# Optimization experiments

Hardware: AMD Instinct MI355X
Metric: run time of the kernel (lower is better)

The kernel has to match this reference:

```python
import jax, jax.numpy as jnp
import numpy as np

N_QUBITS = 4
N_LAYERS = 2
DIM = 1 << N_QUBITS  # 16-dim state vector

# --- fixed (parameter-free) CNOT entangler layers, precomputed as 16x16 permutations ---

def _cnot_perm(c, t):
    M = np.zeros((DIM, DIM), np.complex64)
    for b in range(DIM):
        b2 = b ^ (1 << (N_QUBITS - 1 - t)) if (b >> (N_QUBITS - 1 - c)) & 1 else b
        M[b2, b] = 1.0
    return M

def _entangler(r):
    E = np.eye(DIM, dtype=np.complex64)
    for i in range(N_QUBITS):  # pennylane applies CNOT(i, (i+r)%n) sequentially
        E = _cnot_perm(i, (i + r) % N_QUBITS) @ E
    return E

ENT = [jnp.asarray(_entangler((l % (N_QUBITS - 1)) + 1)) for l in range(N_LAYERS)]
# Z_TABLE[b, w] = <b| Z_w |b>
Z_TABLE = jnp.asarray(np.array([[1.0 - 2.0 * ((b >> (N_QUBITS - 1 - w)) & 1) for w in range(N_QUBITS)] for b in range(DIM)], np.float32))


def _rot(phi, theta, omega):
    # pennylane Rot = RZ(omega) @ RY(theta) @ RZ(phi)
    c = jnp.cos(theta / 2).astype(jnp.complex64)
    s = jnp.sin(theta / 2).astype(jnp.complex64)
    a = jnp.exp(-0.5j * (phi + omega)) * c
    b = -jnp.exp(0.5j * (phi - omega)) * s
    cc = jnp.exp(-0.5j * (phi - omega)) * s
    d = jnp.exp(0.5j * (phi + omega)) * c
    return jnp.stack([jnp.stack([a, b]), jnp.stack([cc, d])])


def _vqc_unitary(weights):
    # weights: [N_LAYERS, N_QUBITS, 3] -> 16x16 unitary for StronglyEntanglingLayers
    U = jnp.eye(DIM, dtype=jnp.complex64)
    for l in range(N_LAYERS):
        R = _rot(weights[l, 0, 0], weights[l, 0, 1], weights[l, 0, 2])
        for q in range(1, N_QUBITS):  # wire 0 is most-significant bit -> left kron factor
            R = jnp.kron(R, _rot(weights[l, q, 0], weights[l, q, 1], weights[l, q, 2]))
        U = ENT[l] @ (R @ U)
    return U


def _vqc(x, weights):
    # x: [..., 4] rotation angles; AngleEmbedding uses RX: RX(a)|0> = [cos(a/2), -i sin(a/2)]
    c = jnp.cos(x / 2).astype(jnp.complex64)
    s = jnp.sin(x / 2).astype(jnp.complex64)
    amp = jnp.stack([c, -1j * s], axis=-1)  # [..., 4, 2]
    psi0 = jnp.einsum('...a,...b,...c,...d->...abcd', amp[..., 0, :], amp[..., 1, :], amp[..., 2, :], amp[..., 3, :])
    psi0 = psi0.reshape(x.shape[:-1] + (DIM,))
    U = _vqc_unitary(weights)
    psi = jnp.einsum('ij,...j->...i', U, psi0)
    probs = psi.real ** 2 + psi.imag ** 2
    return probs @ Z_TABLE  # [..., 4] PauliZ expectation values


def setup_inputs() -> dict:
    key = jax.random.key(0)
    k0, k1, k2, k3 = jax.random.split(key, 4)
    H = 768
    B, S = 8, 2048
    embeddings = jax.random.normal(k0, (B, S, H), dtype=jnp.float32)
    lim = 1.0 / np.sqrt(H)
    Wq = jax.random.normal(k1, (N_QUBITS, H), dtype=jnp.float32) * lim
    Wk = jax.random.normal(k2, (N_QUBITS, H), dtype=jnp.float32) * lim
    bq = jnp.zeros((N_QUBITS,), jnp.float32)
    bk = jnp.zeros((N_QUBITS,), jnp.float32)
    vqc_weights = jax.random.uniform(k3, (N_LAYERS, N_QUBITS, 3), dtype=jnp.float32) * (2.0 * np.pi)
    return {'embeddings': embeddings, 'Wq': Wq, 'bq': bq, 'Wk': Wk, 'bk': bk, 'vqc_weights': vqc_weights}


def reference(embeddings, Wq, bq, Wk, bk, vqc_weights):
    Q = jnp.einsum('bsh,qh->bsq', embeddings, Wq) + bq  # [B,S,4]
    K = jnp.einsum('bsh,qh->bsq', embeddings, Wk) + bk
    Qv = _vqc(Q, vqc_weights)  # [B,S,4]
    Kv = _vqc(K, vqc_weights)
    attn = jax.nn.softmax(jnp.einsum('bsq,btq->bst', Qv, Kv), axis=-1)  # [B,S,S]
    return jnp.einsum('bst,bth->bsh', attn, embeddings)
```

## Files before the change

kernel.cpp:

```cpp
#include <hip/hip_runtime.h>

#define NB 8
#define NS 2048
#define NH 768
#define NPOS (NB*NS)

typedef short short8 __attribute__((ext_vector_type(8)));
typedef float floatx4 __attribute__((ext_vector_type(4)));

__device__ __forceinline__ unsigned pack_bf16(unsigned b0, unsigned b1) {
  return __builtin_amdgcn_perm(b1, b0, 0x07060302u);
}

#define GLOAD_LDS16(gp, lp) __builtin_amdgcn_global_load_lds( \
  (const __attribute__((address_space(1))) unsigned int*)(gp), \
  (__attribute__((address_space(3))) unsigned int*)(lp), 16, 0, 0)

__global__ void build_V_kernel(const float* __restrict__ wts,
                               float* __restrict__ Vre, float* __restrict__ Vim) {
  int j = threadIdx.x;
  if (j >= 16) return;
  float ar[16], ai[16];
#pragma unroll
  for (int i = 0; i < 16; i++) { ar[i] = (i == j) ? 1.f : 0.f; ai[i] = 0.f; }
#pragma unroll
  for (int l = 0; l < 2; l++) {
#pragma unroll
    for (int q = 0; q < 4; q++) {
      float phi = wts[(l*4+q)*3+0];
      float th  = wts[(l*4+q)*3+1];
      float om  = wts[(l*4+q)*3+2];
      float ct = cosf(0.5f*th), st = sinf(0.5f*th);
      float sm = 0.5f*(phi+om), df = 0.5f*(phi-om);
      float cs = cosf(sm), ss = sinf(sm), cd = cosf(df), sd = sinf(df);
      float Ar =  cs*ct, Ai = -ss*ct;
      float Br = -cd*st, Bi = -sd*st;
      float Cr =  cd*st, Ci = -sd*st;
      float Dr =  cs*ct, Di =  ss*ct;
      int pb = 1 << (3-q);
#pragma unroll
      for (int b0 = 0; b0 < 16; b0++) {
        if (b0 & pb) continue;
        int b1 = b0 | pb;
        float xr = ar[b0], xi = ai[b0], yr = ar[b1], yi = ai[b1];
        ar[b0] = Ar*xr - Ai*xi + Br*yr - Bi*yi;
        ai[b0] = Ar*xi + Ai*xr + Br*yi + Bi*yr;
        ar[b1] = Cr*xr - Ci*xi + Dr*yr - Di*yi;
        ai[b1] = Cr*xi + Ci*xr + Dr*yi + Di*yr;
      }
    }
    const int r = (l == 0) ? 1 : 2;
#pragma unroll
    for (int i2 = 0; i2 < 4; i2++) {
      int cb = 1 << (3-i2);
      int tb = 1 << (3-((i2+r)&3));
#pragma unroll
      for (int b0 = 0; b0 < 16; b0++) {
        if ((b0 & cb) && !(b0 & tb)) {
          int b1 = b0 | tb;
          float tr = ar[b0], ti = ai[b0];
          ar[b0] = ar[b1]; ai[b0] = ai[b1];
          ar[b1] = tr;     ai[b1] = ti;
        }
      }
    }
  }
  int pc = __popc((unsigned)j) & 3;
#pragma unroll
  for (int i = 0; i < 16; i++) {
    float vr = ar[i], vi = ai[i], orr, oi;
    if      (pc == 0) { orr =  vr; oi =  vi; }
    else if (pc == 1) { orr =  vi; oi = -vr; }
    else if (pc == 2) { orr = -vr; oi = -vi; }
    else              { orr = -vi; oi =  vr; }
    Vre[i*16+j] = orr;
    Vim[i*16+j] = oi;
  }
}

__global__ __launch_bounds__(256) void proj_vqc_kernel(
    const float* __restrict__ E, const float* __restrict__ Wq, const float* __restrict__ bq,
    const float* __restrict__ Wk, const float* __restrict__ bk,
    const float* __restrict__ Vre, const float* __restrict__ Vim,
    float* __restrict__ Qv, float* __restrict__ Kv) {
  __shared__ __align__(16) float WqL[768*4];
  __shared__ __align__(16) float WkL[768*4];
  __shared__ float Vsh[2][16*17];
  int tid = threadIdx.x;
  for (int idx = tid; idx < 768*4; idx += 256) {
    int e = idx >> 2, w = idx & 3;
    WqL[e*4+w] = Wq[w*768+e];
    WkL[e*4+w] = Wk[w*768+e];
  }
  if (tid < 256) {
    int i = tid >> 4, jj = tid & 15;
    Vsh[0][i*17+jj] = Vre[tid];
    Vsh[1][i*17+jj] = Vim[tid];
  }
  __syncthreads();
  float bqr0=bq[0], bqr1=bq[1], bqr2=bq[2], bqr3=bq[3];
  float bkr0=bk[0], bkr1=bk[1], bkr2=bk[2], bkr3=bk[3];
  int lane = tid & 63;
  int wid  = blockIdx.x*4 + (tid >> 6);
  int nw   = gridDim.x*4;
  int grp  = lane >> 4;
  int i    = lane & 15;
  for (int pos = wid; pos < NPOS; pos += nw) {
    const float* er = E + (size_t)pos*768;
    float pq[4] = {0.f,0.f,0.f,0.f};
    float pk[4] = {0.f,0.f,0.f,0.f};
#pragma unroll
    for (int k2 = 0; k2 < 3; k2++) {
      float4 ev = *(const float4*)(er + lane*4 + 256*k2);
#pragma unroll
      for (int jj = 0; jj < 4; jj++) {
        int e = lane*4 + 256*k2 + jj;
        float evs = (jj==0) ? ev.x : (jj==1) ? ev.y : (jj==2) ? ev.z : ev.w;
        float4 wq4 = *(const float4*)&WqL[e*4];
        float4 wk4 = *(const float4*)&WkL[e*4];
        pq[0] += evs*wq4.x; pq[1] += evs*wq4.y; pq[2] += evs*wq4.z; pq[3] += evs*wq4.w;
        pk[0] += evs*wk4.x; pk[1] += evs*wk4.y; pk[2] += evs*wk4.z; pk[3] += evs*wk4.w;
      }
    }
    float part[8];
#pragma unroll
    for (int w = 0; w < 8; w++) {
      float v = (w < 4) ? pq[w] : pk[w-4];
      v += __shfl_xor(v, 32); v += __shfl_xor(v, 16); v += __shfl_xor(v, 8);
      v += __shfl_xor(v, 4);  v += __shfl_xor(v, 2);  v += __shfl_xor(v, 1);
      part[w] = v;
    }
    if (grp < 2) {
      float a0,a1,a2,a3;
      if (grp == 0) { a0=part[0]+bqr0; a1=part[1]+bqr1; a2=part[2]+bqr2; a3=part[3]+bqr3; }
      else          { a0=part[4]+bkr0; a1=part[5]+bkr1; a2=part[6]+bkr2; a3=part[7]+bkr3; }
      float c0=cosf(0.5f*a0), s0=sinf(0.5f*a0);
      float c1=cosf(0.5f*a1), s1=sinf(0.5f*a1);
      float c2=cosf(0.5f*a2), s2=sinf(0.5f*a2);
      float c3=cosf(0.5f*a3), s3=sinf(0.5f*a3);
      float m[16];
#pragma unroll
      for (int j2 = 0; j2 < 16; j2++) {
        float f0 = (j2 & 8) ? s0 : c0;
        float f1 = (j2 & 4) ? s1 : c1;
        float f2 = (j2 & 2) ? s2 : c2;
        float f3 = (j2 & 1) ? s3 : c3;
        m[j2] = f0*f1*f2*f3;
      }
      float re = 0.f, im = 0.f;
#pragma unroll
      for (int j2 = 0; j2 < 16; j2++) {
        re += Vsh[0][i*17+j2]*m[j2];
        im += Vsh[1][i*17+j2]*m[j2];
      }
      float pr = re*re + im*im;
      float r0 = (i & 8) ? -pr : pr;
      float r1 = (i & 4) ? -pr : pr;
      float r2 = (i & 2) ? -pr : pr;
      float r3 = (i & 1) ? -pr : pr;
#pragma unroll
      for (int off = 8; off >= 1; off >>= 1) {
        r0 += __shfl_xor(r0, off);
        r1 += __shfl_xor(r1, off);
        r2 += __shfl_xor(r2, off);
        r3 += __shfl_xor(r3, off);
      }
      if (i == 0) {
        float* dst = (grp == 0 ? Qv : Kv) + (size_t)pos*4;
        dst[0]=r0; dst[1]=r1; dst[2]=r2; dst[3]=r3;
      }
    }
  }
}

__global__ __launch_bounds__(256) void epre_kernel(
    const float* __restrict__ E, unsigned short* __restrict__ EhiT,
    unsigned short* __restrict__ EloT) {
  int tc = blockIdx.x, hb = blockIdx.y, b = blockIdx.z;
  size_t tbase = ((size_t)((b*6 + hb)*64 + tc)) * 4096;
  const float* Eb = E + (size_t)b*NS*NH + (size_t)tc*32*NH + hb*128;
  int tid = threadIdx.x;
#pragma unroll
  for (int u = 0; u < 2; u++) {
    int unit = tid + 256*u;
    int h2 = unit & 127, q2 = unit >> 7;
    unsigned hi4[4], lo4[4];
#pragma unroll
    for (int jp = 0; jp < 4; jp++) {
      float ea = Eb[(size_t)(q2*8 + 2*jp    )*NH + h2];
      float eb = Eb[(size_t)(q2*8 + 2*jp + 1)*NH + h2];
      unsigned ba = __float_as_uint(ea), bb = __float_as_uint(eb);
      float la = ea - __uint_as_float(ba & 0xFFFF0000u);
      float lb = eb - __uint_as_float(bb & 0xFFFF0000u);
      hi4[jp] = pack_bf16(ba, bb);
      lo4[jp] = pack_bf16(__float_as_uint(la), __float_as_uint(lb));
    }
    int off = h2*32 + ((q2 ^ ((h2>>1)&3))*8);
    *(uint4*)&EhiT[tbase + off] = make_uint4(hi4[0],hi4[1],hi4[2],hi4[3]);
    *(uint4*)&EloT[tbase + off] = make_uint4(lo4[0],lo4[1],lo4[2],lo4[3]);
  }
}

#define BS 128
#define BH 128
#define TK 32

__global__ __launch_bounds__(256, 3) void attn_kernel(
    const float* __restrict__ E, const float* __restrict__ Qv,
    const float* __restrict__ Kv, const unsigned short* __restrict__ EhiT,
    const unsigned short* __restrict__ EloT, float* __restrict__ out) {
  int sblk = blockIdx.x;
  int hblk = blockIdx.y;
  int b    = blockIdx.z;
  int tid  = threadIdx.x;
  int lane = tid & 63;
  int w    = tid >> 6;

  __shared__ __align__(16) unsigned short sAhi[BS*TK];
  __shared__ __align__(16) unsigned short sAlo[BS*TK];
  __shared__ __align__(16) unsigned short sBhi[2][BH*TK];
  __shared__ __align__(16) unsigned short sBlo[2][BH*TK];
  __shared__ __align__(16) float kvf[2][TK][4];
  __shared__ float denp[BS*4];
  __shared__ float dfin[BS];

  const float* Kvb = Kv + (size_t)b*NS*4;
  const unsigned short* tHi = EhiT + ((size_t)(b*6 + hblk)*64) * 4096;
  const unsigned short* tLo = EloT + ((size_t)(b*6 + hblk)*64) * 4096;

  int qw = w, sL = lane;
  floatx4 qv0, qv1;
  {
    const float4 t0 = *(const float4*)&Qv[((size_t)(b*NS + sblk*BS) + sL)*4];
    const float4 t1 = *(const float4*)&Qv[((size_t)(b*NS + sblk*BS) + 64 + sL)*4];
    qv0 = floatx4{t0.x, t0.y, t0.z, t0.w};
    qv1 = floatx4{t1.x, t1.y, t1.z, t1.w};
  }
  float den0 = 0.f, den1 = 0.f;

  int sh = w & 1, hh = w >> 1;
  floatx4 acc[4][4];
#pragma unroll
  for (int i = 0; i < 4; i++)
#pragma unroll
    for (int jt = 0; jt < 4; jt++) acc[i][jt] = floatx4{0.f,0.f,0.f,0.f};

  int m16 = lane & 15, q16 = lane >> 4;
  int cidx = (q16 ^ ((m16 >> 1) & 3)) * 8;

  GLOAD_LDS16(tHi + (size_t)tid*8,        &sBhi[0][tid*8]);
  GLOAD_LDS16(tHi + 2048 + (size_t)tid*8, &sBhi[0][2048 + tid*8]);
  GLOAD_LDS16(tLo + (size_t)tid*8,        &sBlo[0][tid*8]);
  GLOAD_LDS16(tLo + 2048 + (size_t)tid*8, &sBlo[0][2048 + tid*8]);
  if (tid < 32) GLOAD_LDS16(Kvb + tid*4, &kvf[0][0][0] + tid*4);

  for (int tc = 0; tc < NS; tc += TK) {
    int cb = (tc >> 5) & 1;
    __syncthreads();

    {
      unsigned hiA[2][4], loA[2][4];
#pragma unroll
      for (int jp = 0; jp < 4; jp++) {
        float4 ka = *(const float4*)&kvf[cb][qw*8 + 2*jp][0];
        float4 kb = *(const float4*)&kvf[cb][qw*8 + 2*jp + 1][0];
#pragma unroll
        for (int r = 0; r < 2; r++) {
          floatx4 qv = r ? qv1 : qv0;
          float arga = qv.x*ka.x + qv.y*ka.y + qv.z*ka.z + qv.w*ka.w;
          float argb = qv.x*kb.x + qv.y*kb.y + qv.z*kb.z + qv.w*kb.w;
          float pa = __expf(arga), pb = __expf(argb);
          if (r) den1 += pa + pb; else den0 += pa + pb;
          unsigned bpa = __float_as_uint(pa), bpb = __float_as_uint(pb);
          float lpa = pa - __uint_as_float(bpa & 0xFFFF0000u);
          float lpb = pb - __uint_as_float(bpb & 0xFFFF0000u);
          hiA[r][jp] = pack_bf16(bpa, bpb);
          loA[r][jp] = pack_bf16(__float_as_uint(lpa), __float_as_uint(lpb));
        }
      }
#pragma unroll
      for (int r = 0; r < 2; r++) {
        int s = sL + 64*r;
        int off = s*TK + ((qw ^ ((s>>1)&3))*8);
        *(uint4*)&sAhi[off] = make_uint4(hiA[r][0],hiA[r][1],hiA[r][2],hiA[r][3]);
        *(uint4*)&sAlo[off] = make_uint4(loA[r][0],loA[r][1],loA[r][2],loA[r][3]);
      }
    }

    __syncthreads();

    if (tc + TK < NS) {
      int nb = cb ^ 1;
      const unsigned short* nHi = tHi + (size_t)((tc >> 5) + 1) * 4096;
      const unsigned short* nLo = tLo + (size_t)((tc >> 5) + 1) * 4096;
      GLOAD_LDS16(nHi + (size_t)tid*8,        &sBhi[nb][tid*8]);
      GLOAD_LDS16(nHi + 2048 + (size_t)tid*8, &sBhi[nb][2048 + tid*8]);
      GLOAD_LDS16(nLo + (size_t)tid*8,        &sBlo[nb][tid*8]);
      GLOAD_LDS16(nLo + 2048 + (size_t)tid*8, &sBlo[nb][2048 + tid*8]);
      if (tid < 32) GLOAD_LDS16(Kvb + (size_t)(tc+TK)*4 + tid*4, &kvf[nb][0][0] + tid*4);
    }

    short8 bh_[4], bl_[4];
#pragma unroll
    for (int jt = 0; jt < 4; jt++) {
      int hrow = hh*64 + jt*16 + m16;
      bh_[jt] = __builtin_bit_cast(short8, *(const uint4*)&sBhi[cb][hrow*TK + cidx]);
      bl_[jt] = __builtin_bit_cast(short8, *(const uint4*)&sBlo[cb][hrow*TK + cidx]);
    }
#pragma unroll
    for (int i = 0; i < 4; i++) {
      int srow = sh*64 + i*16 + m16;
      short8 ah = __builtin_bit_cast(short8, *(const uint4*)&sAhi[srow*TK + cidx]);
      short8 al = __builtin_bit_cast(short8, *(const uint4*)&sAlo[srow*TK + cidx]);
#pragma unroll
      for (int jt = 0; jt < 4; jt++) {
        acc[i][jt] = __builtin_amdgcn_mfma_f32_16x16x32_bf16(ah, bl_[jt], acc[i][jt], 0, 0, 0);
        acc[i][jt] = __builtin_amdgcn_mfma_f32_16x16x32_bf16(al, bh_[jt], acc[i][jt], 0, 0, 0);
        acc[i][jt] = __builtin_amdgcn_mfma_f32_16x16x32_bf16(ah, bh_[jt], acc[i][jt], 0, 0, 0);
      }
    }
  }

  __syncthreads();
  denp[sL*4 + qw] = den0;
  denp[(64 + sL)*4 + qw] = den1;
  __syncthreads();
  if (tid < BS) {
    dfin[tid] = denp[tid*4] + denp[tid*4+1] + denp[tid*4+2] + denp[tid*4+3];
  }
  __syncthreads();

  float* ob = out + ((size_t)(b*NS + sblk*BS))*NH + hblk*BH;
#pragma unroll
  for (int i = 0; i < 4; i++) {
#pragma unroll
    for (int reg = 0; reg < 4; reg++) {
      int row = q16*4 + reg;
      int s_loc = sh*64 + i*16 + row;
      float invd = 1.0f / dfin[s_loc];
#pragma unroll
      for (int jt = 0; jt < 4; jt++) {
        int h_loc = hh*64 + jt*16 + m16;
        ob[(size_t)s_loc*NH + h_loc] = acc[i][jt][reg] * invd;
      }
    }
  }
}

extern "C" void kernel_launch(void* const* d_in, const int* in_sizes, int n_in,
                              void* d_out, int out_size, void* d_ws, size_t ws_size,
                              hipStream_t stream) {
  const float* E   = (const float*)d_in[0];
  const float* Wq  = (const float*)d_in[1];
  const float* bq  = (const float*)d_in[2];
  const float* Wk  = (const float*)d_in[3];
  const float* bk  = (const float*)d_in[4];
  const float* wts = (const float*)d_in[5];
  float* ws  = (float*)d_ws;
  float* Vre = ws;
  float* Vim = ws + 256;
  float* Qv  = ws + 512;
  float* Kv  = ws + 512 + NPOS*4;
  unsigned short* EhiT = (unsigned short*)(ws + 512 + 2*NPOS*4);
  unsigned short* EloT = EhiT + (size_t)NB*6*64*4096;
  float* out = (float*)d_out;

  build_V_kernel<<<1, 64, 0, stream>>>(wts, Vre, Vim);
  epre_kernel<<<dim3(64, 6, 8), 256, 0, stream>>>(E, EhiT, EloT);
  proj_vqc_kernel<<<1024, 256, 0, stream>>>(E, Wq, bq, Wk, bk, Vre, Vim, Qv, Kv);
  attn_kernel<<<dim3(16, 6, 8), 256, 0, stream>>>(E, Qv, Kv, EhiT, EloT, out);
}
```

Baseline: 323.2 us.

## Precompute softmax numerators once in a separate kernel instead of per H-block

The attention kernel used to recompute exp(Q·K) scores and their bf16 hi/lo split for every one of the six H-blocks. A new pgen_kernel now computes the split probability tiles once, stores them to global memory in the swizzled MFMA layout, and accumulates softmax denominators with atomics after a memset. The attention kernel then streams both the P and E tiles through LDS with async global-to-LDS loads and reorders the MFMA loop so A fragments are held in registers. This trades redundant exp/ALU work for a large extra global write and repeated reads of the P buffer, plus more workspace and an extra launch and memset.

```diff
diff --git a/kernel.cpp b/kernel.cpp
--- a/kernel.cpp
+++ b/kernel.cpp
@@ -201,43 +201,81 @@
   }
 }
 
-#define BS 128
-#define BH 128
-#define TK 32
+__global__ __launch_bounds__(256) void pgen_kernel(
+    const float* __restrict__ Qv, const float* __restrict__ Kv,
+    unsigned short* __restrict__ PhiT, unsigned short* __restrict__ PloT,
+    float* __restrict__ den) {
+  int tq = blockIdx.x, sblk = blockIdx.y, b = blockIdx.z;
+  int tid = threadIdx.x;
+  __shared__ __align__(16) float kvl[256*4];
+  {
+    const float4 v = ((const float4*)(Kv + ((size_t)b*NS + tq*256)*4))[tid];
+    ((float4*)kvl)[tid ^ ((tid >> 3) & 3)] = v;
+  }
+  int s0 = tid >> 2, c = tid & 3;
+  const float* Qb = Qv + ((size_t)b*NS + sblk*128)*4;
+  float4 qv0 = *(const float4*)&Qb[s0*4];
+  float4 qv1 = *(const float4*)&Qb[(64+s0)*4];
+  __syncthreads();
+  float den0 = 0.f, den1 = 0.f;
+  size_t tb = ((size_t)((b*16 + sblk)*64) + tq*8) * 4096;
+  int off0 = s0*32 + ((c ^ ((s0>>1)&3))*8);
+  int off1 = (64+s0)*32 + ((c ^ (((64+s0)>>1)&3))*8);
+#pragma unroll 2
+  for (int tt = 0; tt < 8; tt++) {
+#pragma unroll
+    for (int r = 0; r < 2; r++) {
+      float4 qv = r ? qv1 : qv0;
+      unsigned hi4[4], lo4[4];
+      float dsum = 0.f;
+#pragma unroll
+      for (int jp = 0; jp < 4; jp++) {
+        int La = tt*32 + c*8 + 2*jp;
+        float4 ka = ((const float4*)kvl)[La ^ c];
+        float4 kb = ((const float4*)kvl)[(La+1) ^ c];
+        float arga = qv.x*ka.x + qv.y*ka.y + qv.z*ka.z + qv.w*ka.w;
+        float argb = qv.x*kb.x + qv.y*kb.y + qv.z*kb.z + qv.w*kb.w;
+        float pa = __expf(arga), pb = __expf(argb);
+        dsum += pa + pb;
+        unsigned bpa = __float_as_uint(pa), bpb = __float_as_uint(pb);
+        float lpa = pa - __uint_as_float(bpa & 0xFFFF0000u);
+        float lpb = pb - __uint_as_float(bpb & 0xFFFF0000u);
+        hi4[jp] = pack_bf16(bpa, bpb);
+        lo4[jp] = pack_bf16(__float_as_uint(lpa), __float_as_uint(lpb));
+      }
+      if (r) den1 += dsum; else den0 += dsum;
+      size_t base = tb + (size_t)tt*4096 + (r ? off1 : off0);
+      *(uint4*)&PhiT[base] = make_uint4(hi4[0],hi4[1],hi4[2],hi4[3]);
+      *(uint4*)&PloT[base] = make_uint4(lo4[0],lo4[1],lo4[2],lo4[3]);
+    }
+  }
+  atomicAdd(&den[(size_t)b*NS + sblk*128 + s0], den0);
+  atomicAdd(&den[(size_t)b*NS + sblk*128 + 64 + s0], den1);
+}
+
+#define TKC 32
 
 __global__ __launch_bounds__(256, 3) void attn_kernel(
-    const float* __restrict__ E, const float* __restrict__ Qv,
-    const float* __restrict__ Kv, const unsigned short* __restrict__ EhiT,
-    const unsigned short* __restrict__ EloT, float* __restrict__ out) {
-  int sblk = blockIdx.x;
-  int hblk = blockIdx.y;
+    const unsigned short* __restrict__ PhiT, const unsigned short* __restrict__ PloT,
+    const unsigned short* __restrict__ EhiT, const unsigned short* __restrict__ EloT,
+    const float* __restrict__ den, float* __restrict__ out) {
+  int hblk = blockIdx.x;
+  int sblk = blockIdx.y;
   int b    = blockIdx.z;
   int tid  = threadIdx.x;
   int lane = tid & 63;
   int w    = tid >> 6;
 
-  __shared__ __align__(16) unsigned short sAhi[BS*TK];
-  __shared__ __align__(16) unsigned short sAlo[BS*TK];
-  __shared__ __align__(16) unsigned short sBhi[2][BH*TK];
-  __shared__ __align__(16) unsigned short sBlo[2][BH*TK];
-  __shared__ __align__(16) float kvf[2][TK][4];
-  __shared__ float denp[BS*4];
-  __shared__ float dfin[BS];
-
-  const float* Kvb = Kv + (size_t)b*NS*4;
+  __shared__ __align__(16) unsigned short sAhi[128*TKC];
+  __shared__ __align__(16) unsigned short sAlo[128*TKC];
+  __shared__ __align__(16) unsigned short sBhi[2][128*TKC];
+  __shared__ __align__(16) unsigned short sBlo[2][128*TKC];
+
+  const unsigned short* pHi = PhiT + ((size_t)(b*16 + sblk)*64) * 4096;
+  const unsigned short* pLo = PloT + ((size_t)(b*16 + sblk)*64) * 4096;
   const unsigned short* tHi = EhiT + ((size_t)(b*6 + hblk)*64) * 4096;
   const unsigned short* tLo = EloT + ((size_t)(b*6 + hblk)*64) * 4096;
 
-  int qw = w, sL = lane;
-  floatx4 qv0, qv1;
-  {
-    const float4 t0 = *(const float4*)&Qv[((size_t)(b*NS + sblk*BS) + sL)*4];
-    const float4 t1 = *(const float4*)&Qv[((size_t)(b*NS + sblk*BS) + 64 + sL)*4];
-    qv0 = floatx4{t0.x, t0.y, t0.z, t0.w};
-    qv1 = floatx4{t1.x, t1.y, t1.z, t1.w};
-  }
-  float den0 = 0.f, den1 = 0.f;
-
   int sh = w & 1, hh = w >> 1;
   floatx4 acc[4][4];
 #pragma unroll
@@ -247,97 +285,70 @@
 
   int m16 = lane & 15, q16 = lane >> 4;
   int cidx = (q16 ^ ((m16 >> 1) & 3)) * 8;
-
-  GLOAD_LDS16(tHi + (size_t)tid*8,        &sBhi[0][tid*8]);
-  GLOAD_LDS16(tHi + 2048 + (size_t)tid*8, &sBhi[0][2048 + tid*8]);
-  GLOAD_LDS16(tLo + (size_t)tid*8,        &sBlo[0][tid*8]);
-  GLOAD_LDS16(tLo + 2048 + (size_t)tid*8, &sBlo[0][2048 + tid*8]);
-  if (tid < 32) GLOAD_LDS16(Kvb + tid*4, &kvf[0][0][0] + tid*4);
-
-  for (int tc = 0; tc < NS; tc += TK) {
-    int cb = (tc >> 5) & 1;
+  int t16 = tid * 8;
+
+  GLOAD_LDS16(pHi + t16,        &sAhi[t16]);
+  GLOAD_LDS16(pHi + 2048 + t16, &sAhi[2048 + t16]);
+  GLOAD_LDS16(pLo + t16,        &sAlo[t16]);
+  GLOAD_LDS16(pLo + 2048 + t16, &sAlo[2048 + t16]);
+  GLOAD_LDS16(tHi + t16,        &sBhi[0][t16]);
+  GLOAD_LDS16(tHi + 2048 + t16, &sBhi[0][2048 + t16]);
+  GLOAD_LDS16(tLo + t16,        &sBlo[0][t16]);
+  GLOAD_LDS16(tLo + 2048 + t16, &sBlo[0][2048 + t16]);
+
+  for (int tc = 0; tc < NS; tc += TKC) {
+    int ci = tc >> 5;
+    int cb = ci & 1;
     __syncthreads();
 
-    {
-      unsigned hiA[2][4], loA[2][4];
-#pragma unroll
-      for (int jp = 0; jp < 4; jp++) {
-        float4 ka = *(const float4*)&kvf[cb][qw*8 + 2*jp][0];
-        float4 kb = *(const float4*)&kvf[cb][qw*8 + 2*jp + 1][0];
-#pragma unroll
-        for (int r = 0; r < 2; r++) {
-          floatx4 qv = r ? qv1 : qv0;
-          float arga = qv.x*ka.x + qv.y*ka.y + qv.z*ka.z + qv.w*ka.w;
-          float argb = qv.x*kb.x + qv.y*kb.y + qv.z*kb.z + qv.w*kb.w;
-          float pa = __expf(arga), pb = __expf(argb);
-          if (r) den1 += pa + pb; else den0 += pa + pb;
-          unsigned bpa = __float_as_uint(pa), bpb = __float_as_uint(pb);
-          float lpa = pa - __uint_as_float(bpa & 0xFFFF0000u);
-          float lpb = pb - __uint_as_float(bpb & 0xFFFF0000u);
-          hiA[r][jp] = pack_bf16(bpa, bpb);
-          loA[r][jp] = pack_bf16(__float_as_uint(lpa), __float_as_uint(lpb));
-        }
-      }
-#pragma unroll
-      for (int r = 0; r < 2; r++) {
-        int s = sL + 64*r;
-        int off = s*TK + ((qw ^ ((s>>1)&3))*8);
-        *(uint4*)&sAhi[off] = make_uint4(hiA[r][0],hiA[r][1],hiA[r][2],hiA[r][3]);
-        *(uint4*)&sAlo[off] = make_uint4(loA[r][0],loA[r][1],loA[r][2],loA[r][3]);
-      }
-    }
-
+    short8 ah[4], al[4];
+#pragma unroll
+    for (int i = 0; i < 4; i++) {
+      int srow = sh*64 + i*16 + m16;
+      ah[i] = __builtin_bit_cast(short8, *(const uint4*)&sAhi[srow*TKC + cidx]);
+      al[i] = __builtin_bit_cast(short8, *(const uint4*)&sAlo[srow*TKC + cidx]);
+    }
     __syncthreads();
 
-    if (tc + TK < NS) {
+    if (tc + TKC < NS) {
+      const unsigned short* npHi = pHi + (size_t)(ci+1)*4096;
+      const unsigned short* npLo = pLo + (size_t)(ci+1)*4096;
+      const unsigned short* ntHi = tHi + (size_t)(ci+1)*4096;
+      const unsigned short* ntLo = tLo + (size_t)(ci+1)*4096;
       int nb = cb ^ 1;
-      const unsigned short* nHi = tHi + (size_t)((tc >> 5) + 1) * 4096;
-      const unsigned short* nLo = tLo + (size_t)((tc >> 5) + 1) * 4096;
-      GLOAD_LDS16(nHi + (size_t)tid*8,        &sBhi[nb][tid*8]);
-      GLOAD_LDS16(nHi + 2048 + (size_t)tid*8, &sBhi[nb][2048 + tid*8]);
-      GLOAD_LDS16(nLo + (size_t)tid*8,        &sBlo[nb][tid*8]);
-      GLOAD_LDS16(nLo + 2048 + (size_t)tid*8, &sBlo[nb][2048 + tid*8]);
-      if (tid < 32) GLOAD_LDS16(Kvb + (size_t)(tc+TK)*4 + tid*4, &kvf[nb][0][0] + tid*4);
-    }
-
-    short8 bh_[4], bl_[4];
+      GLOAD_LDS16(npHi + t16,        &sAhi[t16]);
+      GLOAD_LDS16(npHi + 2048 + t16, &sAhi[2048 + t16]);
+      GLOAD_LDS16(npLo + t16,        &sAlo[t16]);
+      GLOAD_LDS16(npLo + 2048 + t16, &sAlo[2048 + t16]);
+      GLOAD_LDS16(ntHi + t16,        &sBhi[nb][t16]);
+      GLOAD_LDS16(ntHi + 2048 + t16, &sBhi[nb][2048 + t16]);
+      GLOAD_LDS16(ntLo + t16,        &sBlo[nb][t16]);
+      GLOAD_LDS16(ntLo + 2048 + t16, &sBlo[nb][2048 + t16]);
+    }
+
 #pragma unroll
     for (int jt = 0; jt < 4; jt++) {
       int hrow = hh*64 + jt*16 + m16;
-      bh_[jt] = __builtin_bit_cast(short8, *(const uint4*)&sBhi[cb][hrow*TK + cidx]);
-      bl_[jt] = __builtin_bit_cast(short8, *(const uint4*)&sBlo[cb][hrow*TK + cidx]);
-    }
-#pragma unroll
-    for (int i = 0; i < 4; i++) {
-      int srow = sh*64 + i*16 + m16;
-      short8 ah = __builtin_bit_cast(short8, *(const uint4*)&sAhi[srow*TK + cidx]);
-      short8 al = __builtin_bit_cast(short8, *(const uint4*)&sAlo[srow*TK + cidx]);
-#pragma unroll
-      for (int jt = 0; jt < 4; jt++) {
-        acc[i][jt] = __builtin_amdgcn_mfma_f32_16x16x32_bf16(ah, bl_[jt], acc[i][jt], 0, 0, 0);
-        acc[i][jt] = __builtin_amdgcn_mfma_f32_16x16x32_bf16(al, bh_[jt], acc[i][jt], 0, 0, 0);
-        acc[i][jt] = __builtin_amdgcn_mfma_f32_16x16x32_bf16(ah, bh_[jt], acc[i][jt], 0, 0, 0);
-      }
-    }
-  }
-
-  __syncthreads();
-  denp[sL*4 + qw] = den0;
-  denp[(64 + sL)*4 + qw] = den1;
-  __syncthreads();
-  if (tid < BS) {
-    dfin[tid] = denp[tid*4] + denp[tid*4+1] + denp[tid*4+2] + denp[tid*4+3];
-  }
-  __syncthreads();
-
-  float* ob = out + ((size_t)(b*NS + sblk*BS))*NH + hblk*BH;
+      short8 bh_ = __builtin_bit_cast(short8, *(const uint4*)&sBhi[cb][hrow*TKC + cidx]);
+      short8 bl_ = __builtin_bit_cast(short8, *(const uint4*)&sBlo[cb][hrow*TKC + cidx]);
+#pragma unroll
+      for (int i = 0; i < 4; i++) {
+        acc[i][jt] = __builtin_amdgcn_mfma_f32_16x16x32_bf16(ah[i], bl_, acc[i][jt], 0, 0, 0);
+        acc[i][jt] = __builtin_amdgcn_mfma_f32_16x16x32_bf16(al[i], bh_, acc[i][jt], 0, 0, 0);
+        acc[i][jt] = __builtin_amdgcn_mfma_f32_16x16x32_bf16(ah[i], bh_, acc[i][jt], 0, 0, 0);
+      }
+    }
+  }
+
+  const float* den_g = den + (size_t)b*NS + sblk*128;
+  float* ob = out + ((size_t)(b*NS + sblk*128))*NH + hblk*128;
 #pragma unroll
   for (int i = 0; i < 4; i++) {
 #pragma unroll
     for (int reg = 0; reg < 4; reg++) {
       int row = q16*4 + reg;
       int s_loc = sh*64 + i*16 + row;
-      float invd = 1.0f / dfin[s_loc];
+      float invd = 1.0f / den_g[s_loc];
 #pragma unroll
       for (int jt = 0; jt < 4; jt++) {
         int h_loc = hh*64 + jt*16 + m16;
@@ -360,13 +371,18 @@
   float* Vre = ws;
   float* Vim = ws + 256;
   float* Qv  = ws + 512;
-  float* Kv  = ws + 512 + NPOS*4;
-  unsigned short* EhiT = (unsigned short*)(ws + 512 + 2*NPOS*4);
+  float* Kv  = Qv + (size_t)NPOS*4;
+  float* den = Kv + (size_t)NPOS*4;
+  unsigned short* EhiT = (unsigned short*)(den + NPOS);
   unsigned short* EloT = EhiT + (size_t)NB*6*64*4096;
+  unsigned short* PhiT = EloT + (size_t)NB*6*64*4096;
+  unsigned short* PloT = PhiT + (size_t)NB*16*64*4096;
   float* out = (float*)d_out;
 
   build_V_kernel<<<1, 64, 0, stream>>>(wts, Vre, Vim);
   epre_kernel<<<dim3(64, 6, 8), 256, 0, stream>>>(E, EhiT, EloT);
   proj_vqc_kernel<<<1024, 256, 0, stream>>>(E, Wq, bq, Wk, bk, Vre, Vim, Qv, Kv);
-  attn_kernel<<<dim3(16, 6, 8), 256, 0, stream>>>(E, Qv, Kv, EhiT, EloT, out);
-}
+  hipMemsetAsync(den, 0, (size_t)NPOS*sizeof(float), stream);
+  pgen_kernel<<<dim3(8, 16, 8), 256, 0, stream>>>(Qv, Kv, PhiT, PloT, den);
+  attn_kernel<<<dim3(6, 16, 8), 256, 0, stream>>>(PhiT, PloT, EhiT, EloT, den, out);
+}
```

New measurement: 364.7 us. +12.9%, slower.
